# Performance work log

Measured on AMD Instinct MI355X. Metric: run time of the kernel, lower is better.

The kernel has to match this reference:

```python
import jax, jax.numpy as jnp
import numpy as np

B, T, D = 2, 2048, 2048
H, L = 16, 64
Hd = D // H  # 128
SCALE = 1.0 / np.sqrt(L).astype(np.float32)


def apply_rope(q, k, freqs):
    # q, k: [B, T, H, Hd]; freqs: [T, Hd//2] angles (theta)
    cos = jnp.cos(freqs)[None, :, None, :]  # [1,T,1,Hd/2]
    sin = jnp.sin(freqs)[None, :, None, :]

    def rot(t):
        tr = t.reshape(*t.shape[:-1], Hd // 2, 2)
        a, b = tr[..., 0], tr[..., 1]
        return jnp.stack([a * cos - b * sin, a * sin + b * cos], axis=-1).reshape(t.shape)

    return rot(q), rot(k)


def setup_inputs() -> dict:
    key = jax.random.key(0)
    ks = jax.random.split(key, 16)

    def w(k, shape):
        return jax.random.normal(k, shape, jnp.float32) * 0.02

    x = jax.random.normal(ks[0], (B, T, D), jnp.float32)
    # RoPE angles: theta[t, i] = t / 10000^(2i/Hd)
    inv = 1.0 / (10000.0 ** (jnp.arange(0, Hd, 2, dtype=jnp.float32) / Hd))
    freqs = jnp.arange(T, dtype=jnp.float32)[:, None] * inv[None, :]  # [T, Hd/2]
    # additive causal mask
    mask = jnp.where(jnp.tril(jnp.ones((T, T), bool)), 0.0, -1e9).astype(jnp.float32)

    return dict(
        x=x, freqs=freqs, mask=mask,
        Wq=w(ks[1], (D, D)), bq=jnp.zeros((D,), jnp.float32),
        Wk=w(ks[2], (D, D)), bk=jnp.zeros((D,), jnp.float32),
        Wv=w(ks[3], (D, D)), bv=jnp.zeros((D,), jnp.float32),
        Wo=w(ks[4], (D, D)), bo=jnp.zeros((D,), jnp.float32),
        Wcq=w(ks[5], (Hd, L)), bcq=jnp.zeros((L,), jnp.float32),
        Wck=w(ks[6], (Hd, L)), bck=jnp.zeros((L,), jnp.float32),
        Wcv=w(ks[7], (Hd, L)), bcv=jnp.zeros((L,), jnp.float32),
        Wd=w(ks[8], (L, Hd)), bd=jnp.zeros((Hd,), jnp.float32),
    )


def reference(x, freqs, mask, Wq, bq, Wk, bk, Wv, bv, Wo, bo,
              Wcq, bcq, Wck, bck, Wcv, bcv, Wd, bd):
    b, t, d = x.shape
    q = (x @ Wq + bq).reshape(b, t, H, Hd)
    k = (x @ Wk + bk).reshape(b, t, H, Hd)
    v = (x @ Wv + bv).reshape(b, t, H, Hd)

    q, k = apply_rope(q, k, freqs)

    # per-head latent compression [B,T,H,L]
    q_lat = jnp.einsum('bthd,dl->bthl', q, Wcq) + bcq
    k_lat = jnp.einsum('bthd,dl->bthl', k, Wck) + bck
    v_lat = jnp.einsum('bthd,dl->bthl', v, Wcv) + bcv

    scores = jnp.einsum('bthl,bshl->bhts', q_lat, k_lat) * SCALE
    scores = scores + mask[None, None, :, :]
    attn = jax.nn.softmax(scores, axis=-1)

    out = jnp.einsum('bhts,bshl->bthl', attn, v_lat)  # [B,T,H,L]
    out = jnp.einsum('bthl,lk->bthk', out, Wd) + bd    # decompress -> [B,T,H,Hd]
    out = out.reshape(b, t, d)
    return out @ Wo + bo
```

## Files before the change

### kernel.cpp

```cpp
#include <hip/hip_runtime.h>
#include <hip/hip_bf16.h>

static constexpr int Bsz = 2;
static constexpr int Tn  = 2048;
static constexpr int Dn  = 2048;
static constexpr int Hn  = 16;
static constexpr int Ln  = 64;
static constexpr int Hd  = 128;
static constexpr float SL2E = 0.125f * 1.44269504088896f;

typedef short short8 __attribute__((ext_vector_type(8)));
typedef float f32x4 __attribute__((ext_vector_type(4)));
typedef unsigned short ushort8 __attribute__((ext_vector_type(8)));
typedef unsigned short ushort4v __attribute__((ext_vector_type(4)));
typedef _Float16 half8 __attribute__((ext_vector_type(8)));
typedef unsigned short u16;

__device__ inline u16 f16_rne(float f) {
  _Float16 h = (_Float16)f;
  union { _Float16 h; u16 u; } x; x.h = h;
  return x.u;
}
__device__ inline float f16_to_f(u16 u) {
  union { u16 u; _Float16 h; } x; x.u = u;
  return (float)x.h;
}

#define GL(g, l) __builtin_amdgcn_global_load_lds(                     \
    (const __attribute__((address_space(1))) void*)(g),                \
    (__attribute__((address_space(3))) void*)(l), 16, 0, 0)

__global__ void split_h(const float* __restrict__ A, u16* __restrict__ O,
                        int nblk, int Kd) {
  int b = blockIdx.x * 256 + threadIdx.x;
  if (b >= nblk) return;
  int perRow = Kd >> 3;
  int m = b / perRow, gb = b - m * perRow;
  int w = gb >> 2, g = gb & 3;
  const float* src = A + (size_t)m * Kd + (w << 5) + (g << 2);
  float4 v0 = *(const float4*)src;
  float4 v1 = *(const float4*)(src + 16);
  float e[8] = {v0.x, v0.y, v0.z, v0.w, v1.x, v1.y, v1.z, v1.w};
  ushort8 o;
#pragma unroll
  for (int j = 0; j < 8; ++j) o[j] = f16_rne(e[j]);
  *(ushort8*)(O + (size_t)b * 8) = o;
}

__global__ __launch_bounds__(256) void transpose_h(
    const float* __restrict__ W, u16* __restrict__ Th, int Kd, int Nd) {
  __shared__ float t[32][33];
  int k0 = blockIdx.x * 32, n0 = blockIdx.y * 32;
  int i = threadIdx.x;
  {
    int kk = i >> 3, nn = (i & 7) << 2;
    float4 v = *(const float4*)&W[(size_t)(k0 + kk) * Nd + n0 + nn];
    t[kk][nn] = v.x; t[kk][nn + 1] = v.y; t[kk][nn + 2] = v.z; t[kk][nn + 3] = v.w;
  }
  __syncthreads();
  int n = i >> 3, t2 = i & 7;
  int g = t2 >> 1, h = t2 & 1;
  int kbase = h * 16 + g * 4;
  ushort4v o;
#pragma unroll
  for (int j = 0; j < 4; ++j) o[j] = f16_rne(t[kbase + j][n]);
  *(ushort4v*)(Th + (size_t)(n0 + n) * Kd + k0 + t2 * 4) = o;
}

__global__ __launch_bounds__(256) void fold64(
    const float* __restrict__ A, int lda, int a_bx, int a_by,
    const float* __restrict__ B, int ldb, int b_bx, int b_by,
    float* __restrict__ C, int ldc, int c_bx, int c_by) {
  __shared__ float a_lds[64][132];
  __shared__ float b_lds[128][64];
  const int bx = blockIdx.x, by = blockIdx.y, tid = threadIdx.x;
  A += (size_t)bx * a_bx + (size_t)by * a_by;
  B += (size_t)bx * b_bx + (size_t)by * b_by;
  C += (size_t)bx * c_bx + (size_t)by * c_by;
  for (int i = tid; i < 64 * 32; i += 256) {
    int r = i >> 5, c4 = (i & 31) << 2;
    *(float4*)&a_lds[r][c4] = *(const float4*)&A[(size_t)r * lda + c4];
  }
  for (int i = tid; i < 128 * 16; i += 256) {
    int r = i >> 4, c4 = (i & 15) << 2;
    *(float4*)&b_lds[r][c4] = *(const float4*)&B[(size_t)r * ldb + c4];
  }
  __syncthreads();
  const int r = tid >> 2, l0 = (tid & 3) << 4;
  float acc[16] = {};
  for (int k = 0; k < 128; ++k) {
    float av = a_lds[r][k];
    const float* bp = &b_lds[k][l0];
#pragma unroll
    for (int j = 0; j < 16; ++j) acc[j] += av * bp[j];
  }
#pragma unroll
  for (int j4 = 0; j4 < 4; ++j4)
    *(float4*)&C[(size_t)r * ldc + l0 + j4 * 4] = *(float4*)&acc[j4 * 4];
}

__global__ void bias_prep(const float* __restrict__ bv, const float* __restrict__ Wcv,
                          const float* __restrict__ bcv, const float* __restrict__ bd,
                          const float* __restrict__ Wo, const float* __restrict__ bo,
                          float* __restrict__ bias_vf, float* __restrict__ bias_out) {
  int idx = blockIdx.x * 256 + threadIdx.x;
  if (idx < 1024) {
    int h = idx >> 6, l = idx & 63;
    float s = bcv[l];
    for (int j = 0; j < 128; ++j) s += bv[h * 128 + j] * Wcv[j * 64 + l];
    bias_vf[idx] = s;
  } else if (idx < 3072) {
    int n = idx - 1024;
    float s = bo[n];
    for (int k = 0; k < 2048; ++k) s += bd[k & 127] * Wo[(size_t)k * 2048 + n];
    bias_out[n] = s;
  }
}

__global__ __launch_bounds__(256) void gemm_qkv(
    const u16* __restrict__ Af, const u16* __restrict__ Bf,
    u16* __restrict__ cQ, u16* __restrict__ cK, u16* __restrict__ cV,
    const float* __restrict__ bq, const float* __restrict__ bk,
    const float* __restrict__ bvf, int K) {
  __shared__ u16 s[2][2][128 * 64];
  const int tid = threadIdx.x;
  const int lane = tid & 63;
  const int w = tid >> 6, wr = w >> 1, wc = w & 1;
  const int l15 = lane & 15, lg = lane >> 4;
  const int row0 = blockIdx.y * 128, col0 = blockIdx.x * 128;

  const int sr = tid >> 3, sq = tid & 7;
  const int sg = sq ^ (sr & 7);
  size_t aoff[4], boff[4];
#pragma unroll
  for (int j = 0; j < 4; ++j) {
    aoff[j] = (size_t)(row0 + j * 32 + sr) * K + sg * 8;
    boff[j] = (size_t)(col0 + j * 32 + sr) * K + sg * 8;
  }

  f32x4 acc[4][4];
#pragma unroll
  for (int i2 = 0; i2 < 4; ++i2)
#pragma unroll
    for (int j2 = 0; j2 < 4; ++j2) acc[i2][j2] = (f32x4){0.f, 0.f, 0.f, 0.f};

  int fa[4][2], fb[4][2];
#pragma unroll
  for (int mi = 0; mi < 4; ++mi) {
    int ra = wr * 64 + mi * 16 + l15;
    int rb = wc * 64 + mi * 16 + l15;
#pragma unroll
    for (int kk = 0; kk < 2; ++kk) {
      fa[mi][kk] = ra * 128 + (((kk * 4 + lg) ^ (ra & 7)) << 4);
      fb[mi][kk] = rb * 128 + (((kk * 4 + lg) ^ (rb & 7)) << 4);
    }
  }

#pragma unroll
  for (int j = 0; j < 4; ++j) {
    GL(Af + aoff[j], (char*)&s[0][0][0] + j * 4096 + tid * 16);
    GL(Bf + boff[j], (char*)&s[0][1][0] + j * 4096 + tid * 16);
  }
  int cur = 0;
  for (int k0 = 0; k0 < K; k0 += 64) {
    __syncthreads();
    if (k0 + 64 < K) {
      const int nb = cur ^ 1;
#pragma unroll
      for (int j = 0; j < 4; ++j) {
        GL(Af + aoff[j] + k0 + 64, (char*)&s[nb][0][0] + j * 4096 + tid * 16);
        GL(Bf + boff[j] + k0 + 64, (char*)&s[nb][1][0] + j * 4096 + tid * 16);
      }
    }
#pragma unroll
    for (int kk = 0; kk < 2; ++kk) {
      half8 a[4], b[4];
#pragma unroll
      for (int mi = 0; mi < 4; ++mi) {
        a[mi] = *(const half8*)((const char*)&s[cur][0][0] + fa[mi][kk]);
        b[mi] = *(const half8*)((const char*)&s[cur][1][0] + fb[mi][kk]);
      }
#pragma unroll
      for (int mi = 0; mi < 4; ++mi)
#pragma unroll
        for (int ni = 0; ni < 4; ++ni)
          acc[mi][ni] = __builtin_amdgcn_mfma_f32_16x16x32_f16(a[mi], b[ni], acc[mi][ni], 0, 0, 0);
    }
    cur ^= 1;
  }
  u16* Cp; const float* bp; int ldc, cl0;
  if (col0 < 2048)      { Cp = cQ; bp = bq;  ldc = 2048; cl0 = col0; }
  else if (col0 < 4096) { Cp = cK; bp = bk;  ldc = 2048; cl0 = col0 - 2048; }
  else                  { Cp = cV; bp = bvf; ldc = 1024; cl0 = col0 - 4096; }
#pragma unroll
  for (int ni = 0; ni < 4; ++ni) {
    int c = cl0 + wc * 64 + ni * 16 + l15;
    float bias = bp[c];
#pragma unroll
    for (int mi = 0; mi < 4; ++mi) {
      int rr = row0 + wr * 64 + mi * 16 + lg * 4;
#pragma unroll
      for (int r = 0; r < 4; ++r)
        Cp[(size_t)(rr + r) * ldc + c] = f16_rne(acc[mi][ni][r] + bias);
    }
  }
}

__global__ __launch_bounds__(256) void gemm_f16(
    const u16* __restrict__ Af, const u16* __restrict__ Bf,
    const float* __restrict__ bias, float* __restrict__ C,
    int M, int N, int K) {
  __shared__ u16 s[2][2][128 * 32];
  const int tid = threadIdx.x;
  const int lane = tid & 63;
  const int w = tid >> 6, wr = w >> 1, wc = w & 1;
  const int row0 = blockIdx.y * 128, col0 = blockIdx.x * 128;

  const int sr = tid >> 2, sq = tid & 3;
  const int sg = sq ^ ((sr >> 1) & 3);
  const size_t aoff0 = (size_t)(row0 + sr) * K + sg * 8;
  const size_t aoff1 = (size_t)(row0 + sr + 64) * K + sg * 8;
  const size_t boff0 = (size_t)(col0 + sr) * K + sg * 8;
  const size_t boff1 = (size_t)(col0 + sr + 64) * K + sg * 8;
  const int ldst0 = tid * 16, ldst1 = (tid + 256) * 16;

  f32x4 acc[4][4];
#pragma unroll
  for (int i2 = 0; i2 < 4; ++i2)
#pragma unroll
    for (int j2 = 0; j2 < 4; ++j2) acc[i2][j2] = (f32x4){0.f, 0.f, 0.f, 0.f};

  int fa[4], fb[4];
#pragma unroll
  for (int mi = 0; mi < 4; ++mi) {
    int ra = wr * 64 + mi * 16 + (lane & 15);
    fa[mi] = ra * 64 + (((lane >> 4) ^ ((ra >> 1) & 3)) << 4);
    int rb = wc * 64 + mi * 16 + (lane & 15);
    fb[mi] = rb * 64 + (((lane >> 4) ^ ((rb >> 1) & 3)) << 4);
  }

  GL(Af + aoff0, (char*)&s[0][0][0] + ldst0);
  GL(Af + aoff1, (char*)&s[0][0][0] + ldst1);
  GL(Bf + boff0, (char*)&s[0][1][0] + ldst0);
  GL(Bf + boff1, (char*)&s[0][1][0] + ldst1);
  int cur = 0;
  for (int k0 = 0; k0 < K; k0 += 32) {
    __syncthreads();
    if (k0 + 32 < K) {
      const int nb = cur ^ 1;
      GL(Af + aoff0 + k0 + 32, (char*)&s[nb][0][0] + ldst0);
      GL(Af + aoff1 + k0 + 32, (char*)&s[nb][0][0] + ldst1);
      GL(Bf + boff0 + k0 + 32, (char*)&s[nb][1][0] + ldst0);
      GL(Bf + boff1 + k0 + 32, (char*)&s[nb][1][0] + ldst1);
    }
    half8 a[4], b[4];
#pragma unroll
    for (int mi = 0; mi < 4; ++mi) {
      a[mi] = *(const half8*)((const char*)&s[cur][0][0] + fa[mi]);
      b[mi] = *(const half8*)((const char*)&s[cur][1][0] + fb[mi]);
    }
#pragma unroll
    for (int mi = 0; mi < 4; ++mi)
#pragma unroll
      for (int ni = 0; ni < 4; ++ni)
        acc[mi][ni] = __builtin_amdgcn_mfma_f32_16x16x32_f16(a[mi], b[ni], acc[mi][ni], 0, 0, 0);
    cur ^= 1;
  }
#pragma unroll
  for (int ni = 0; ni < 4; ++ni) {
    int c = col0 + wc * 64 + ni * 16 + (lane & 15);
    float bv = bias[c];
#pragma unroll
    for (int mi = 0; mi < 4; ++mi) {
      int rr = row0 + wr * 64 + mi * 16 + ((lane >> 4) << 2);
#pragma unroll
      for (int r = 0; r < 4; ++r)
        C[(size_t)(rr + r) * N + c] = acc[mi][ni][r] + bv;
    }
  }
}

__global__ __launch_bounds__(256) void compress_qk_mfma(
    const u16* __restrict__ src, const u16* __restrict__ WcT,
    const float* __restrict__ bc, const float* __restrict__ freqs,
    u16* __restrict__ dst) {
  __shared__ u16 q_lds[64 * 128];
  __shared__ u16 w_lds[64 * 128];
  const int tid = threadIdx.x;
  const int lane = tid & 63;
  const int w = tid >> 6;
  const int t0 = blockIdx.x * 64;
  const int bh = blockIdx.y, b = bh >> 4, h = bh & 15;

#pragma unroll
  for (int j = 0; j < 4; ++j) {
    int idx = tid + j * 256;
    int row = idx >> 4, slot = idx & 15;
    GL(WcT + (size_t)row * 128 + (size_t)(slot ^ (row & 7)) * 8,
       (char*)w_lds + idx * 16);
  }
  const int r = tid >> 2, seg = tid & 3;
  const u16* qp = src + ((size_t)(b * Tn + t0 + r)) * Dn + h * 128 + seg * 32;
  const float* fp = freqs + (size_t)(t0 + r) * 64 + seg * 16;
  float fr[16];
#pragma unroll
  for (int j = 0; j < 4; ++j) *(float4*)&fr[4 * j] = ((const float4*)fp)[j];
#pragma unroll
  for (int j = 0; j < 8; ++j) {
    ushort4v uv = *(const ushort4v*)(qp + 4 * j);
    float e0 = f16_to_f(uv[0]), e1 = f16_to_f(uv[1]);
    float e2 = f16_to_f(uv[2]), e3 = f16_to_f(uv[3]);
    float s0, c0, s1, c1;
    sincosf(fr[2 * j], &s0, &c0);
    sincosf(fr[2 * j + 1], &s1, &c1);
    ushort4v u;
    u[0] = f16_rne(e0 * c0 - e1 * s0);
    u[1] = f16_rne(e0 * s0 + e1 * c0);
    u[2] = f16_rne(e2 * c1 - e3 * s1);
    u[3] = f16_rne(e2 * s1 + e3 * c1);
    int slot = seg * 4 + (j & 3);
    *(ushort4v*)((char*)q_lds + r * 256 + ((slot ^ (r & 7)) << 4) + (j >> 2) * 8) = u;
  }
  __syncthreads();
  const int l15 = lane & 15, lg = lane >> 4;
  const int arow = w * 16 + l15;
  half8 af[4];
#pragma unroll
  for (int ks = 0; ks < 4; ++ks)
    af[ks] = *(const half8*)((const char*)q_lds + arow * 256 +
                             (((ks * 4 + lg) ^ (arow & 7)) << 4));
  f32x4 acc[4];
#pragma unroll
  for (int ni = 0; ni < 4; ++ni) acc[ni] = (f32x4){0.f, 0.f, 0.f, 0.f};
#pragma unroll
  for (int ni = 0; ni < 4; ++ni) {
    const int brow = ni * 16 + l15;
#pragma unroll
    for (int ks = 0; ks < 4; ++ks) {
      half8 bf = *(const half8*)((const char*)w_lds + brow * 256 +
                                 (((ks * 4 + lg) ^ (brow & 7)) << 4));
      acc[ni] = __builtin_amdgcn_mfma_f32_16x16x32_f16(af[ks], bf, acc[ni], 0, 0, 0);
    }
  }
  __syncthreads();
#pragma unroll
  for (int ni = 0; ni < 4; ++ni) {
    int lat = ni * 16 + l15;
    float bcv = bc[lat];
    int p = (lat & 32) + ((lat >> 2) & 3) * 8 + ((lat >> 4) & 1) * 4 + (lat & 3);
#pragma unroll
    for (int reg = 0; reg < 4; ++reg)
      q_lds[w * 1024 + (lg * 4 + reg) * 64 + p] = f16_rne(acc[ni][reg] + bcv);
  }
  __syncthreads();
#pragma unroll
  for (int j = 0; j < 2; ++j) {
    int idx = tid + j * 256;
    int row = idx >> 3, c8 = idx & 7;
    ushort8 val = *(const ushort8*)&q_lds[row * 64 + c8 * 8];
    *(ushort8*)(dst + ((size_t)bh * Tn + t0 + row) * 64 + c8 * 8) = val;
  }
}

__global__ __launch_bounds__(256) void transpose_v(
    const u16* __restrict__ vlat, u16* __restrict__ vlatT) {
  __shared__ u16 o_lds[64][64];
  const int tid = threadIdx.x;
  const int t0 = blockIdx.x * 64;
  const int bh = blockIdx.y, b = bh >> 4, h = bh & 15;
  const int tt = tid >> 2, lseg = tid & 3;
  const u16* vp = vlat + (size_t)(b * Tn + t0 + tt) * 1024 + h * 64 + lseg * 16;
#pragma unroll
  for (int g = 0; g < 4; ++g) {
    ushort4v u = *(const ushort4v*)(vp + g * 4);
    *(ushort4v*)&o_lds[tt][lseg * 16 + ((g ^ (tt & 3)) << 2)] = u;
  }
  __syncthreads();
  const int lat = tid >> 2, tseg = tid & 3;
  const int tw = tseg >> 1, h4 = tseg & 1;
  u16 vals[16];
#pragma unroll
  for (int i = 0; i < 16; ++i)
    vals[i] = o_lds[tseg * 16 + i][lat ^ ((i & 3) << 2)];
  u16* dp = vlatT + ((size_t)bh * 64 + lat) * Tn + t0 + tw * 32 + h4 * 4;
#pragma unroll
  for (int g = 0; g < 4; ++g) {
    ushort4v u = {vals[g * 4 + 0], vals[g * 4 + 1], vals[g * 4 + 2], vals[g * 4 + 3]};
    *(ushort4v*)(dp + g * 8) = u;
  }
}

__global__ __launch_bounds__(256) void attn_mfma(
    const u16* __restrict__ qlat, const u16* __restrict__ klat,
    const u16* __restrict__ vlatT, u16* __restrict__ oh) {
  __shared__ u16 Ks[64 * 72];
  __shared__ u16 Vs[64 * 72];
  __shared__ u16 Os[128][72];
  const int tid = threadIdx.x;
  const int lane = tid & 63;
  const int w = tid >> 6;
  const int bh = blockIdx.y, b = bh >> 4, h = bh & 15;
  const int q0 = (int)(gridDim.x - 1 - blockIdx.x) * 128;
  const int qw = q0 + w * 32;
  const u16* ql = qlat + (size_t)bh * Tn * 64;
  const u16* kl = klat + (size_t)bh * Tn * 64;
  const u16* vt = vlatT + (size_t)bh * 64 * Tn;
  const int l15 = lane & 15, lg = lane >> 4;

  half8 qf[2][2];
#pragma unroll
  for (int nf = 0; nf < 2; ++nf)
#pragma unroll
    for (int ks = 0; ks < 2; ++ks)
      qf[nf][ks] = *(const half8*)(const void*)(ql + (size_t)(qw + nf * 16 + l15) * 64 + (ks * 4 + lg) * 8);

  f32x4 accO[4][2];
#pragma unroll
  for (int mi = 0; mi < 4; ++mi)
#pragma unroll
    for (int nf = 0; nf < 2; ++nf) accO[mi][nf] = (f32x4){0.f, 0.f, 0.f, 0.f};
  float mrow[2] = {-1e30f, -1e30f}, lrow[2] = {0.f, 0.f};

  const int srow = tid >> 2, spair = tid & 3;
  u16* ksw = &Ks[srow * 72 + spair * 16];
  u16* vsw = &Vs[srow * 72 + spair * 16];
  const u16* kgp = kl + (size_t)srow * 64 + spair * 16;
  const u16* vgp = vt + (size_t)srow * Tn + spair * 16;

  ushort8 kr0 = *(const ushort8*)(kgp);
  ushort8 kr1 = *(const ushort8*)(kgp + 8);
  ushort8 vr0 = *(const ushort8*)(vgp);
  ushort8 vr1 = *(const ushort8*)(vgp + 8);

  const int ntiles = q0 / 64 + 2;
  for (int kt = 0; kt < ntiles; ++kt) {
    const int k0 = kt * 64;
    __syncthreads();
    *(ushort8*)ksw       = kr0;
    *(ushort8*)(ksw + 8) = kr1;
    *(ushort8*)vsw       = vr0;
    *(ushort8*)(vsw + 8) = vr1;
    __syncthreads();
    {
      int kn = k0 + 64; kn = kn > (int)Tn - 64 ? (int)Tn - 64 : kn;
      kr0 = *(const ushort8*)(kgp + (size_t)kn * 64);
      kr1 = *(const ushort8*)(kgp + (size_t)kn * 64 + 8);
      vr0 = *(const ushort8*)(vgp + kn);
      vr1 = *(const ushort8*)(vgp + kn + 8);
    }
    if (k0 <= qw + 31) {
      f32x4 s4[4][2];
#pragma unroll
      for (int mi = 0; mi < 4; ++mi) {
        s4[mi][0] = (f32x4){0.f, 0.f, 0.f, 0.f};
        s4[mi][1] = (f32x4){0.f, 0.f, 0.f, 0.f};
      }
      __builtin_amdgcn_s_setprio(1);
#pragma unroll
      for (int ks = 0; ks < 2; ++ks) {
        half8 kf[4];
#pragma unroll
        for (int mi = 0; mi < 4; ++mi)
          kf[mi] = *(const half8*)(const void*)&Ks[(mi * 16 + l15) * 72 + (ks * 4 + lg) * 8];
#pragma unroll
        for (int mi = 0; mi < 4; ++mi) {
          s4[mi][0] = __builtin_amdgcn_mfma_f32_16x16x32_f16(kf[mi], qf[0][ks], s4[mi][0], 0, 0, 0);
          s4[mi][1] = __builtin_amdgcn_mfma_f32_16x16x32_f16(kf[mi], qf[1][ks], s4[mi][1], 0, 0, 0);
        }
      }
      __builtin_amdgcn_s_setprio(0);
      ushort8 pf[2][2];
#pragma unroll
      for (int nf = 0; nf < 2; ++nf) {
        const int qidx = qw + nf * 16 + l15;
        float p[4][4];
        float tmax = -1e30f;
#pragma unroll
        for (int mi = 0; mi < 4; ++mi)
#pragma unroll
          for (int rr = 0; rr < 4; ++rr) {
            int kv = k0 + mi * 16 + lg * 4 + rr;
            float v = s4[mi][nf][rr] * SL2E;
            if (kv > qidx) v = -1e30f;
            p[mi][rr] = v;
            tmax = fmaxf(tmax, v);
          }
        tmax = fmaxf(tmax, __shfl_xor(tmax, 16));
        tmax = fmaxf(tmax, __shfl_xor(tmax, 32));
        float mnew = fmaxf(mrow[nf], tmax);
        float alpha = exp2f(mrow[nf] - mnew);
        mrow[nf] = mnew;
        float psum = 0.f;
        u16 ph[4][4];
#pragma unroll
        for (int mi = 0; mi < 4; ++mi)
#pragma unroll
          for (int rr = 0; rr < 4; ++rr) {
            float e = exp2f(p[mi][rr] - mnew);
            u16 hb = f16_rne(e);
            psum += f16_to_f(hb);
            ph[mi][rr] = hb;
          }
        psum += __shfl_xor(psum, 16);
        psum += __shfl_xor(psum, 32);
        lrow[nf] = lrow[nf] * alpha + psum;
#pragma unroll
        for (int mi = 0; mi < 4; ++mi)
#pragma unroll
          for (int rr = 0; rr < 4; ++rr) accO[mi][nf][rr] *= alpha;
#pragma unroll
        for (int ks = 0; ks < 2; ++ks) {
          ushort8 f;
#pragma unroll
          for (int rr = 0; rr < 4; ++rr) {
            f[rr]     = ph[2 * ks][rr];
            f[4 + rr] = ph[2 * ks + 1][rr];
          }
          pf[nf][ks] = f;
        }
      }
      __builtin_amdgcn_s_setprio(1);
#pragma unroll
      for (int ks = 0; ks < 2; ++ks) {
        half8 vf[4];
#pragma unroll
        for (int mi = 0; mi < 4; ++mi)
          vf[mi] = *(const half8*)(const void*)&Vs[(mi * 16 + l15) * 72 + (ks * 4 + lg) * 8];
#pragma unroll
        for (int mi = 0; mi < 4; ++mi) {
          accO[mi][0] = __builtin_amdgcn_mfma_f32_16x16x32_f16(vf[mi], *(const half8*)&pf[0][ks], accO[mi][0], 0, 0, 0);
          accO[mi][1] = __builtin_amdgcn_mfma_f32_16x16x32_f16(vf[mi], *(const half8*)&pf[1][ks], accO[mi][1], 0, 0, 0);
        }
      }
      __builtin_amdgcn_s_setprio(0);
    }
  }
  __syncthreads();
#pragma unroll
  for (int nf = 0; nf < 2; ++nf) {
    float inv = 1.f / lrow[nf];
    int qloc = w * 32 + nf * 16 + l15;
#pragma unroll
    for (int mi = 0; mi < 4; ++mi) {
      int pbase = (mi >> 1) * 32 + lg * 8 + (mi & 1) * 4;
      ushort4v u;
#pragma unroll
      for (int rr = 0; rr < 4; ++rr) u[rr] = f16_rne(accO[mi][nf][rr] * inv);
      *(ushort4v*)&Os[qloc][pbase] = u;
    }
  }
  __syncthreads();
  {
    int rid = tid >> 1, hf = tid & 1;
    int q = q0 + rid;
    u16* dstp = oh + ((size_t)(b * Tn + q)) * 1024 + h * 64 + hf * 32;
#pragma unroll
    for (int g = 0; g < 4; ++g)
      *(ushort8*)(dstp + g * 8) = *(const ushort8*)&Os[rid][hf * 32 + g * 8];
  }
}

extern "C" void kernel_launch(void* const* d_in, const int* in_sizes, int n_in,
                              void* d_out, int out_size, void* d_ws, size_t ws_size,
                              hipStream_t stream) {
  const float* x     = (const float*)d_in[0];
  const float* freqs = (const float*)d_in[1];
  const float* Wq  = (const float*)d_in[3];  const float* bq  = (const float*)d_in[4];
  const float* Wk  = (const float*)d_in[5];  const float* bk  = (const float*)d_in[6];
  const float* Wv  = (const float*)d_in[7];  const float* bv  = (const float*)d_in[8];
  const float* Wo  = (const float*)d_in[9];  const float* bo  = (const float*)d_in[10];
  const float* Wcq = (const float*)d_in[11]; const float* bcq = (const float*)d_in[12];
  const float* Wck = (const float*)d_in[13]; const float* bck = (const float*)d_in[14];
  const float* Wcv = (const float*)d_in[15]; const float* bcv = (const float*)d_in[16];
  const float* Wd  = (const float*)d_in[17]; const float* bd  = (const float*)d_in[18];
  float* out = (float*)d_out;

  const size_t BT = (size_t)Bsz * Tn;
  const size_t nQ = BT * Dn;
  const size_t nL = BT * Hn * Ln;
  const size_t nWT = (size_t)5120 * 2048;

  char* ws = (char*)d_ws;
  u16* xf   = (u16*)ws;
  u16* WTf  = xf + nQ;
  float* Wvf = (float*)(WTf + nWT);
  u16* Qh   = (u16*)(Wvf + (size_t)2048 * 1024);
  u16* Kh   = Qh + nQ;
  u16* vlat = Kh + nQ;
  float* bias_vf  = (float*)(vlat + (size_t)4096 * 1024);
  float* bias_out = bias_vf + 1024;
  u16* qlat  = (u16*)(bias_out + 2048);
  u16* klat  = qlat + nL;
  u16* vlatT = klat + nL;
  u16* oh = (u16*)(vlatT + nL);
  float* Wdo = (float*)(oh + (size_t)4096 * 1024);
  u16* WdoT = (u16*)(Wdo + (size_t)1024 * 2048);
  u16* WcqT = WdoT + (size_t)2048 * 1024;
  u16* WckT = WcqT + (size_t)64 * 128;

  dim3 blk(256);
  int nblkA = (int)(nQ / 8);

  split_h<<<(nblkA + 255) / 256, blk, 0, stream>>>(x, xf, nblkA, Dn);
  fold64<<<dim3(32, 16), blk, 0, stream>>>(Wv, 2048, 64 * 2048, 128,
                                           Wcv, 64, 0, 0,
                                           Wvf, 1024, 64 * 1024, 64);
  transpose_h<<<dim3(64, 64), blk, 0, stream>>>(Wq, WTf, 2048, 2048);
  transpose_h<<<dim3(64, 64), blk, 0, stream>>>(Wk, WTf + (size_t)2048 * 2048, 2048, 2048);
  transpose_h<<<dim3(64, 32), blk, 0, stream>>>(Wvf, WTf + (size_t)4096 * 2048, 2048, 1024);
  transpose_h<<<dim3(4, 2), blk, 0, stream>>>(Wcq, WcqT, 128, 64);
  transpose_h<<<dim3(4, 2), blk, 0, stream>>>(Wck, WckT, 128, 64);
  bias_prep<<<12, blk, 0, stream>>>(bv, Wcv, bcv, bd, Wo, bo, bias_vf, bias_out);

  gemm_qkv<<<dim3(40, 32), blk, 0, stream>>>(xf, WTf, Qh, Kh, vlat,
                                             bq, bk, bias_vf, 2048);

  dim3 gc(Tn / 64, Bsz * Hn);
  compress_qk_mfma<<<gc, blk, 0, stream>>>(Qh, WcqT, bcq, freqs, qlat);
  compress_qk_mfma<<<gc, blk, 0, stream>>>(Kh, WckT, bck, freqs, klat);
  transpose_v<<<gc, blk, 0, stream>>>(vlat, vlatT);

  attn_mfma<<<dim3(Tn / 128, Bsz * Hn), blk, 0, stream>>>(qlat, klat, vlatT, oh);

  fold64<<<dim3(32, 16), blk, 0, stream>>>(Wd, 128, 0, 0,
                                           Wo, 2048, 64, 128 * 2048,
                                           Wdo, 2048, 64, 64 * 2048);
  transpose_h<<<dim3(32, 64), blk, 0, stream>>>(Wdo, WdoT, 1024, 2048);
  gemm_f16<<<dim3(16, 32), blk, 0, stream>>>(oh, WdoT, bias_out, out, (int)BT, 2048, 1024);
}
```

Before: 388.6 us.

## Shrink attention query tile, add lazy rescale, and deepen output GEMM K-tile

The attention kernel now handles 64 queries per block (16 per wave) instead of 128, which doubles the grid and removes the idle causal-skip branches. It masks only on the diagonal tile and rescales the running max lazily, only when the new max exceeds the old by more than 8 (log2 units). Separately, the output GEMM moves from a 32-wide to a 64-wide K step with a new XOR swizzle, halving loop iterations and barriers at the cost of twice the LDS. The lazy rescale lets unnormalised fp16 probabilities grow up to 2^8, a small overflow/precision risk, and the smaller attention tile loads K/V tiles twice as often per query.

```diff
diff --git a/kernel.cpp b/kernel.cpp
--- a/kernel.cpp
+++ b/kernel.cpp
@@ -210,19 +210,21 @@
     const u16* __restrict__ Af, const u16* __restrict__ Bf,
     const float* __restrict__ bias, float* __restrict__ C,
     int M, int N, int K) {
-  __shared__ u16 s[2][2][128 * 32];
+  __shared__ u16 s[2][2][128 * 64];
   const int tid = threadIdx.x;
   const int lane = tid & 63;
   const int w = tid >> 6, wr = w >> 1, wc = w & 1;
+  const int l15 = lane & 15, lg = lane >> 4;
   const int row0 = blockIdx.y * 128, col0 = blockIdx.x * 128;
 
-  const int sr = tid >> 2, sq = tid & 3;
-  const int sg = sq ^ ((sr >> 1) & 3);
-  const size_t aoff0 = (size_t)(row0 + sr) * K + sg * 8;
-  const size_t aoff1 = (size_t)(row0 + sr + 64) * K + sg * 8;
-  const size_t boff0 = (size_t)(col0 + sr) * K + sg * 8;
-  const size_t boff1 = (size_t)(col0 + sr + 64) * K + sg * 8;
-  const int ldst0 = tid * 16, ldst1 = (tid + 256) * 16;
+  const int sr = tid >> 3, sq = tid & 7;
+  const int sg = sq ^ (sr & 7);
+  size_t aoff[4], boff[4];
+#pragma unroll
+  for (int j = 0; j < 4; ++j) {
+    aoff[j] = (size_t)(row0 + j * 32 + sr) * K + sg * 8;
+    boff[j] = (size_t)(col0 + j * 32 + sr) * K + sg * 8;
+  }
 
   f32x4 acc[4][4];
 #pragma unroll
@@ -230,49 +232,57 @@
 #pragma unroll
     for (int j2 = 0; j2 < 4; ++j2) acc[i2][j2] = (f32x4){0.f, 0.f, 0.f, 0.f};
 
-  int fa[4], fb[4];
+  int fa[4][2], fb[4][2];
 #pragma unroll
   for (int mi = 0; mi < 4; ++mi) {
-    int ra = wr * 64 + mi * 16 + (lane & 15);
-    fa[mi] = ra * 64 + (((lane >> 4) ^ ((ra >> 1) & 3)) << 4);
-    int rb = wc * 64 + mi * 16 + (lane & 15);
-    fb[mi] = rb * 64 + (((lane >> 4) ^ ((rb >> 1) & 3)) << 4);
-  }
-
-  GL(Af + aoff0, (char*)&s[0][0][0] + ldst0);
-  GL(Af + aoff1, (char*)&s[0][0][0] + ldst1);
-  GL(Bf + boff0, (char*)&s[0][1][0] + ldst0);
-  GL(Bf + boff1, (char*)&s[0][1][0] + ldst1);
+    int ra = wr * 64 + mi * 16 + l15;
+    int rb = wc * 64 + mi * 16 + l15;
+#pragma unroll
+    for (int kk = 0; kk < 2; ++kk) {
+      fa[mi][kk] = ra * 128 + (((kk * 4 + lg) ^ (ra & 7)) << 4);
+      fb[mi][kk] = rb * 128 + (((kk * 4 + lg) ^ (rb & 7)) << 4);
+    }
+  }
+
+#pragma unroll
+  for (int j = 0; j < 4; ++j) {
+    GL(Af + aoff[j], (char*)&s[0][0][0] + j * 4096 + tid * 16);
+    GL(Bf + boff[j], (char*)&s[0][1][0] + j * 4096 + tid * 16);
+  }
   int cur = 0;
-  for (int k0 = 0; k0 < K; k0 += 32) {
+  for (int k0 = 0; k0 < K; k0 += 64) {
     __syncthreads();
-    if (k0 + 32 < K) {
+    if (k0 + 64 < K) {
       const int nb = cur ^ 1;
-      GL(Af + aoff0 + k0 + 32, (char*)&s[nb][0][0] + ldst0);
-      GL(Af + aoff1 + k0 + 32, (char*)&s[nb][0][0] + ldst1);
-      GL(Bf + boff0 + k0 + 32, (char*)&s[nb][1][0] + ldst0);
-      GL(Bf + boff1 + k0 + 32, (char*)&s[nb][1][0] + ldst1);
-    }
-    half8 a[4], b[4];
+#pragma unroll
+      for (int j = 0; j < 4; ++j) {
+        GL(Af + aoff[j] + k0 + 64, (char*)&s[nb][0][0] + j * 4096 + tid * 16);
+        GL(Bf + boff[j] + k0 + 64, (char*)&s[nb][1][0] + j * 4096 + tid * 16);
+      }
+    }
+#pragma unroll
+    for (int kk = 0; kk < 2; ++kk) {
+      half8 a[4], b[4];
+#pragma unroll
+      for (int mi = 0; mi < 4; ++mi) {
+        a[mi] = *(const half8*)((const char*)&s[cur][0][0] + fa[mi][kk]);
+        b[mi] = *(const half8*)((const char*)&s[cur][1][0] + fb[mi][kk]);
+      }
+#pragma unroll
+      for (int mi = 0; mi < 4; ++mi)
+#pragma unroll
+        for (int ni = 0; ni < 4; ++ni)
+          acc[mi][ni] = __builtin_amdgcn_mfma_f32_16x16x32_f16(a[mi], b[ni], acc[mi][ni], 0, 0, 0);
+    }
+    cur ^= 1;
+  }
+#pragma unroll
+  for (int ni = 0; ni < 4; ++ni) {
+    int c = col0 + wc * 64 + ni * 16 + l15;
+    float bv = bias[c];
 #pragma unroll
     for (int mi = 0; mi < 4; ++mi) {
-      a[mi] = *(const half8*)((const char*)&s[cur][0][0] + fa[mi]);
-      b[mi] = *(const half8*)((const char*)&s[cur][1][0] + fb[mi]);
-    }
-#pragma unroll
-    for (int mi = 0; mi < 4; ++mi)
-#pragma unroll
-      for (int ni = 0; ni < 4; ++ni)
-        acc[mi][ni] = __builtin_amdgcn_mfma_f32_16x16x32_f16(a[mi], b[ni], acc[mi][ni], 0, 0, 0);
-    cur ^= 1;
-  }
-#pragma unroll
-  for (int ni = 0; ni < 4; ++ni) {
-    int c = col0 + wc * 64 + ni * 16 + (lane & 15);
-    float bv = bias[c];
-#pragma unroll
-    for (int mi = 0; mi < 4; ++mi) {
-      int rr = row0 + wr * 64 + mi * 16 + ((lane >> 4) << 2);
+      int rr = row0 + wr * 64 + mi * 16 + lg * 4;
 #pragma unroll
       for (int r = 0; r < 4; ++r)
         C[(size_t)(rr + r) * N + c] = acc[mi][ni][r] + bv;
@@ -395,31 +405,27 @@
     const u16* __restrict__ vlatT, u16* __restrict__ oh) {
   __shared__ u16 Ks[64 * 72];
   __shared__ u16 Vs[64 * 72];
-  __shared__ u16 Os[128][72];
+  __shared__ u16 Os[64][72];
   const int tid = threadIdx.x;
   const int lane = tid & 63;
   const int w = tid >> 6;
   const int bh = blockIdx.y, b = bh >> 4, h = bh & 15;
-  const int q0 = (int)(gridDim.x - 1 - blockIdx.x) * 128;
-  const int qw = q0 + w * 32;
+  const int q0 = (int)(gridDim.x - 1 - blockIdx.x) * 64;
+  const int qw = q0 + w * 16;
   const u16* ql = qlat + (size_t)bh * Tn * 64;
   const u16* kl = klat + (size_t)bh * Tn * 64;
   const u16* vt = vlatT + (size_t)bh * 64 * Tn;
   const int l15 = lane & 15, lg = lane >> 4;
 
-  half8 qf[2][2];
-#pragma unroll
-  for (int nf = 0; nf < 2; ++nf)
-#pragma unroll
-    for (int ks = 0; ks < 2; ++ks)
-      qf[nf][ks] = *(const half8*)(const void*)(ql + (size_t)(qw + nf * 16 + l15) * 64 + (ks * 4 + lg) * 8);
-
-  f32x4 accO[4][2];
-#pragma unroll
-  for (int mi = 0; mi < 4; ++mi)
-#pragma unroll
-    for (int nf = 0; nf < 2; ++nf) accO[mi][nf] = (f32x4){0.f, 0.f, 0.f, 0.f};
-  float mrow[2] = {-1e30f, -1e30f}, lrow[2] = {0.f, 0.f};
+  half8 qf[2];
+#pragma unroll
+  for (int ks = 0; ks < 2; ++ks)
+    qf[ks] = *(const half8*)(const void*)(ql + (size_t)(qw + l15) * 64 + (ks * 4 + lg) * 8);
+
+  f32x4 accO[4];
+#pragma unroll
+  for (int mi = 0; mi < 4; ++mi) accO[mi] = (f32x4){0.f, 0.f, 0.f, 0.f};
+  float mrow = -1e30f, lrow = 0.f;
 
   const int srow = tid >> 2, spair = tid & 3;
   u16* ksw = &Ks[srow * 72 + spair * 16];
@@ -432,7 +438,7 @@
   ushort8 vr0 = *(const ushort8*)(vgp);
   ushort8 vr1 = *(const ushort8*)(vgp + 8);
 
-  const int ntiles = q0 / 64 + 2;
+  const int ntiles = q0 / 64 + 1;
   for (int kt = 0; kt < ntiles; ++kt) {
     const int k0 = kt * 64;
     __syncthreads();
@@ -448,115 +454,104 @@
       vr0 = *(const ushort8*)(vgp + kn);
       vr1 = *(const ushort8*)(vgp + kn + 8);
     }
-    if (k0 <= qw + 31) {
-      f32x4 s4[4][2];
-#pragma unroll
-      for (int mi = 0; mi < 4; ++mi) {
-        s4[mi][0] = (f32x4){0.f, 0.f, 0.f, 0.f};
-        s4[mi][1] = (f32x4){0.f, 0.f, 0.f, 0.f};
+    f32x4 s4[4];
+#pragma unroll
+    for (int mi = 0; mi < 4; ++mi) s4[mi] = (f32x4){0.f, 0.f, 0.f, 0.f};
+    __builtin_amdgcn_s_setprio(1);
+#pragma unroll
+    for (int ks = 0; ks < 2; ++ks) {
+      half8 kf[4];
+#pragma unroll
+      for (int mi = 0; mi < 4; ++mi)
+        kf[mi] = *(const half8*)(const void*)&Ks[(mi * 16 + l15) * 72 + (ks * 4 + lg) * 8];
+#pragma unroll
+      for (int mi = 0; mi < 4; ++mi)
+        s4[mi] = __builtin_amdgcn_mfma_f32_16x16x32_f16(kf[mi], qf[ks], s4[mi], 0, 0, 0);
+    }
+    __builtin_amdgcn_s_setprio(0);
+    const bool needmask = (kt == ntiles - 1);
+    const int qidx = qw + l15;
+    float p[4][4];
+    float tmax = -1e30f;
+#pragma unroll
+    for (int mi = 0; mi < 4; ++mi)
+#pragma unroll
+      for (int rr = 0; rr < 4; ++rr) {
+        float v = s4[mi][rr] * SL2E;
+        if (needmask && (k0 + mi * 16 + lg * 4 + rr > qidx)) v = -1e30f;
+        p[mi][rr] = v;
+        tmax = fmaxf(tmax, v);
       }
-      __builtin_amdgcn_s_setprio(1);
-#pragma unroll
-      for (int ks = 0; ks < 2; ++ks) {
-        half8 kf[4];
-#pragma unroll
-        for (int mi = 0; mi < 4; ++mi)
-          kf[mi] = *(const half8*)(const void*)&Ks[(mi * 16 + l15) * 72 + (ks * 4 + lg) * 8];
-#pragma unroll
-        for (int mi = 0; mi < 4; ++mi) {
-          s4[mi][0] = __builtin_amdgcn_mfma_f32_16x16x32_f16(kf[mi], qf[0][ks], s4[mi][0], 0, 0, 0);
-          s4[mi][1] = __builtin_amdgcn_mfma_f32_16x16x32_f16(kf[mi], qf[1][ks], s4[mi][1], 0, 0, 0);
-        }
+    tmax = fmaxf(tmax, __shfl_xor(tmax, 16));
+    tmax = fmaxf(tmax, __shfl_xor(tmax, 32));
+    if (!__all(tmax - mrow <= 8.f)) {
+      float mnew = fmaxf(mrow, tmax);
+      float alpha = exp2f(mrow - mnew);
+      lrow *= alpha;
+#pragma unroll
+      for (int mi = 0; mi < 4; ++mi)
+#pragma unroll
+        for (int rr = 0; rr < 4; ++rr) accO[mi][rr] *= alpha;
+      mrow = mnew;
+    }
+    float psum = 0.f;
+    u16 ph[4][4];
+#pragma unroll
+    for (int mi = 0; mi < 4; ++mi)
+#pragma unroll
+      for (int rr = 0; rr < 4; ++rr) {
+        float e = exp2f(p[mi][rr] - mrow);
+        u16 hb = f16_rne(e);
+        psum += f16_to_f(hb);
+        ph[mi][rr] = hb;
       }
-      __builtin_amdgcn_s_setprio(0);
-      ushort8 pf[2][2];
-#pragma unroll
-      for (int nf = 0; nf < 2; ++nf) {
-        const int qidx = qw + nf * 16 + l15;
-        float p[4][4];
-        float tmax = -1e30f;
-#pragma unroll
-        for (int mi = 0; mi < 4; ++mi)
-#pragma unroll
-          for (int rr = 0; rr < 4; ++rr) {
-            int kv = k0 + mi * 16 + lg * 4 + rr;
-            float v = s4[mi][nf][rr] * SL2E;
-            if (kv > qidx) v = -1e30f;
-            p[mi][rr] = v;
-            tmax = fmaxf(tmax, v);
-          }
-        tmax = fmaxf(tmax, __shfl_xor(tmax, 16));
-        tmax = fmaxf(tmax, __shfl_xor(tmax, 32));
-        float mnew = fmaxf(mrow[nf], tmax);
-        float alpha = exp2f(mrow[nf] - mnew);
-        mrow[nf] = mnew;
-        float psum = 0.f;
-        u16 ph[4][4];
-#pragma unroll
-        for (int mi = 0; mi < 4; ++mi)
-#pragma unroll
-          for (int rr = 0; rr < 4; ++rr) {
-            float e = exp2f(p[mi][rr] - mnew);
-            u16 hb = f16_rne(e);
-            psum += f16_to_f(hb);
-            ph[mi][rr] = hb;
-          }
-        psum += __shfl_xor(psum, 16);
-        psum += __shfl_xor(psum, 32);
-        lrow[nf] = lrow[nf] * alpha + psum;
-#pragma unroll
-        for (int mi = 0; mi < 4; ++mi)
-#pragma unroll
-          for (int rr = 0; rr < 4; ++rr) accO[mi][nf][rr] *= alpha;
-#pragma unroll
-        for (int ks = 0; ks < 2; ++ks) {
-          ushort8 f;
-#pragma unroll
-          for (int rr = 0; rr < 4; ++rr) {
-            f[rr]     = ph[2 * ks][rr];
-            f[4 + rr] = ph[2 * ks + 1][rr];
-          }
-          pf[nf][ks] = f;
-        }
+    psum += __shfl_xor(psum, 16);
+    psum += __shfl_xor(psum, 32);
+    lrow += psum;
+    ushort8 pf[2];
+#pragma unroll
+    for (int ks = 0; ks < 2; ++ks) {
+      ushort8 f;
+#pragma unroll
+      for (int rr = 0; rr < 4; ++rr) {
+        f[rr]     = ph[2 * ks][rr];
+        f[4 + rr] = ph[2 * ks + 1][rr];
       }
-      __builtin_amdgcn_s_setprio(1);
-#pragma unroll
-      for (int ks = 0; ks < 2; ++ks) {
-        half8 vf[4];
-#pragma unroll
-        for (int mi = 0; mi < 4; ++mi)
-          vf[mi] = *(const half8*)(const void*)&Vs[(mi * 16 + l15) * 72 + (ks * 4 + lg) * 8];
-#pragma unroll
-        for (int mi = 0; mi < 4; ++mi) {
-          accO[mi][0] = __builtin_amdgcn_mfma_f32_16x16x32_f16(vf[mi], *(const half8*)&pf[0][ks], accO[mi][0], 0, 0, 0);
-          accO[mi][1] = __builtin_amdgcn_mfma_f32_16x16x32_f16(vf[mi], *(const half8*)&pf[1][ks], accO[mi][1], 0, 0, 0);
-        }
-      }
-      __builtin_amdgcn_s_setprio(0);
-    }
-  }
-  __syncthreads();
-#pragma unroll
-  for (int nf = 0; nf < 2; ++nf) {
-    float inv = 1.f / lrow[nf];
-    int qloc = w * 32 + nf * 16 + l15;
+      pf[ks] = f;
+    }
+    __builtin_amdgcn_s_setprio(1);
+#pragma unroll
+    for (int ks = 0; ks < 2; ++ks) {
+      half8 vf[4];
+#pragma unroll
+      for (int mi = 0; mi < 4; ++mi)
+        vf[mi] = *(const half8*)(const void*)&Vs[(mi * 16 + l15) * 72 + (ks * 4 + lg) * 8];
+#pragma unroll
+      for (int mi = 0; mi < 4; ++mi)
+        accO[mi] = __builtin_amdgcn_mfma_f32_16x16x32_f16(vf[mi], *(const half8*)&pf[ks], accO[mi], 0, 0, 0);
+    }
+    __builtin_amdgcn_s_setprio(0);
+  }
+  __syncthreads();
+  {
+    float inv = 1.f / lrow;
+    int qloc = w * 16 + l15;
 #pragma unroll
     for (int mi = 0; mi < 4; ++mi) {
       int pbase = (mi >> 1) * 32 + lg * 8 + (mi & 1) * 4;
       ushort4v u;
 #pragma unroll
-      for (int rr = 0; rr < 4; ++rr) u[rr] = f16_rne(accO[mi][nf][rr] * inv);
+      for (int rr = 0; rr < 4; ++rr) u[rr] = f16_rne(accO[mi][rr] * inv);
       *(ushort4v*)&Os[qloc][pbase] = u;
     }
   }
   __syncthreads();
   {
-    int rid = tid >> 1, hf = tid & 1;
-    int q = q0 + rid;
-    u16* dstp = oh + ((size_t)(b * Tn + q)) * 1024 + h * 64 + hf * 32;
-#pragma unroll
-    for (int g = 0; g < 4; ++g)
-      *(ushort8*)(dstp + g * 8) = *(const ushort8*)&Os[rid][hf * 32 + g * 8];
+    int rid = tid >> 2, seg = tid & 3;
+    u16* dstp = oh + ((size_t)(b * Tn + q0 + rid)) * 1024 + h * 64 + seg * 16;
+#pragma unroll
+    for (int g = 0; g < 2; ++g)
+      *(ushort8*)(dstp + g * 8) = *(const ushort8*)&Os[rid][seg * 16 + g * 8];
   }
 }
 
@@ -620,7 +615,7 @@
   compress_qk_mfma<<<gc, blk, 0, stream>>>(Kh, WckT, bck, freqs, klat);
   transpose_v<<<gc, blk, 0, stream>>>(vlat, vlatT);
 
-  attn_mfma<<<dim3(Tn / 128, Bsz * Hn), blk, 0, stream>>>(qlat, klat, vlatT, oh);
+  attn_mfma<<<dim3(Tn / 64, Bsz * Hn), blk, 0, stream>>>(qlat, klat, vlatT, oh);
 
   fold64<<<dim3(32, 16), blk, 0, stream>>>(Wd, 128, 0, 0,
                                            Wo, 2048, 64, 128 * 2048,
```

Result: faster. 363.0 us (-6.6%).
